# Optimization experiments

Hardware: AMD Instinct MI355X
Metric: run time of the kernel (lower is better)

The kernel has to match this reference:

```python
import jax, jax.numpy as jnp
import numpy as np

N_FFT = 64
FFT_STRIDE = 32
WINDOW_LENGTH = 1024
STRIDE = 128
FS = 2000.0


def _hann_nonperiodic(n):
    # torch.hann_window(n, periodic=False)
    k = jnp.arange(n, dtype=jnp.float32)
    return 0.5 * (1.0 - jnp.cos(2.0 * jnp.pi * k / (n - 1)))


def setup_inputs() -> dict:
    key = jax.random.key(0)
    inputs = jax.random.normal(key, (16, 16, 40000), dtype=jnp.float32)
    return {"inputs": inputs}


def reference(inputs) -> jnp.ndarray:
    B, C, T = inputs.shape
    num_freqs = N_FFT // 2 + 1
    window = _hann_nonperiodic(N_FFT)
    wnorm = jnp.linalg.norm(window)

    # --- STFT (center=False, onesided, complex), matching torch.stft ---
    x = inputs.reshape(B * C, T)
    num_frames = (T - N_FFT) // FFT_STRIDE + 1  # 1249
    frame_idx = jnp.arange(num_frames)[:, None] * FFT_STRIDE + jnp.arange(N_FFT)[None, :]
    frames = x[:, frame_idx] * window  # (BC, frames, n_fft)
    spec = jnp.fft.rfft(frames, axis=-1) / wnorm  # (BC, frames, F) complex64
    spec = jnp.swapaxes(spec, 1, 2)  # (BC, F, frames)

    # --- unfold over time frames into MPF windows ---
    ws = WINDOW_LENGTH // FFT_STRIDE  # 32
    step = STRIDE // FFT_STRIDE  # 4
    num_windows = (num_frames - ws) // step + 1  # 305
    widx = jnp.arange(num_windows)[:, None] * step + jnp.arange(ws)[None, :]
    spec_w = spec[:, :, widx]  # (BC, F, W, ws)
    spec_w = spec_w.reshape(B, C, num_freqs, num_windows, ws)
    spec_w = jnp.transpose(spec_w, (0, 3, 2, 1, 4))  # (B, W, F, C, ws)

    # --- cross-spectral density, |.|^2 ---
    csd = jnp.einsum("bwfcs,bwfds->bwfcd", spec_w, jnp.conj(spec_w)) / ws
    csd = csd.real ** 2 + csd.imag ** 2  # (B, W, F, C, C) real, PSD

    # --- log-eigen reconstruction ---
    eigvals, eigvecs = jnp.linalg.eigh(csd)
    eigvals = jnp.nan_to_num(jnp.log(eigvals), nan=0.0, neginf=0.0)
    out = (eigvecs * eigvals[..., None, :]) @ jnp.swapaxes(eigvecs, -1, -2)
    # (B, W, F, C, C) -> (B, F, C, C, W)
    return jnp.transpose(out, (0, 2, 3, 4, 1))
```

## Files before the change

kernel.cpp:

```cpp
#include <hip/hip_runtime.h>
#include <math.h>

#define NFRAMES 1249
#define NFREQ   33
#define NWIN    305
#define NCH     16
#define T_IN    40000
#define NSWEEP  8

__global__ __launch_bounds__(256) void kspec(const float* __restrict__ x,
                                             float2* __restrict__ spec) {
    __shared__ float2 twid[64];
    __shared__ float  win[64];
    int tid = threadIdx.x;
    if (tid < 64) {
        const float PI2 = 6.28318530717958647692f;
        float ang = (PI2 / 64.0f) * (float)tid;
        twid[tid] = make_float2(cosf(ang), -sinf(ang));
        float wv  = 0.5f * (1.0f - cosf((PI2 / 63.0f) * (float)tid));
        win[tid]  = wv * (1.0f / sqrtf(23.625f));
    }
    __syncthreads();

    int fl = tid & 15;
    int c  = tid >> 4;
    int b  = blockIdx.y;
    int frame = blockIdx.x * 16 + fl;
    if (frame >= NFRAMES) return;

    const float* xp = x + (size_t)(b * 16 + c) * T_IN + (size_t)frame * 32;
    float xw[64];
    #pragma unroll
    for (int k = 0; k < 16; k++) {
        float4 v = reinterpret_cast<const float4*>(xp)[k];
        xw[4*k+0] = v.x * win[4*k+0];
        xw[4*k+1] = v.y * win[4*k+1];
        xw[4*k+2] = v.z * win[4*k+2];
        xw[4*k+3] = v.w * win[4*k+3];
    }
    for (int f = 0; f < NFREQ; f++) {
        float re = 0.0f, im = 0.0f;
        #pragma unroll
        for (int n = 0; n < 64; n++) {
            float2 tw = twid[(f * n) & 63];
            re = fmaf(xw[n], tw.x, re);
            im = fmaf(xw[n], tw.y, im);
        }
        spec[((size_t)(b * NFREQ + f) * NFRAMES + frame) * NCH + c] = make_float2(re, im);
    }
}

__global__ __launch_bounds__(256) void keig(const float2* __restrict__ spec,
                                            float* __restrict__ outC, int direct) {
    __shared__ float Gs[16][16][17];
    __shared__ float Hs[16][16][17];
    int tid  = threadIdx.x;
    int lane = tid & 63;
    int matl = tid >> 4;
    int t    = tid & 15;
    int mat  = blockIdx.x * 16 + matl;
    int wwin = mat % NWIN;
    int bf   = mat / NWIN;

    const float2* zb = spec + ((size_t)bf * NFRAMES + (size_t)wwin * 4) * NCH;

    float cr[16], ci[16];
    #pragma unroll
    for (int c2 = 0; c2 < 16; c2++) { cr[c2] = 0.0f; ci[c2] = 0.0f; }
    for (int chunk = 0; chunk < 4; chunk++) {
        float zx[8], zy[8];
        #pragma unroll
        for (int s = 0; s < 8; s++) {
            float2 z = zb[(size_t)(chunk * 8 + s) * NCH + t];
            zx[s] = z.x; zy[s] = z.y;
        }
        #pragma unroll
        for (int c2 = 0; c2 < 16; c2++) {
            int src = (lane & 48) | c2;
            #pragma unroll
            for (int s = 0; s < 8; s++) {
                float zcx = __shfl(zx[s], src);
                float zcy = __shfl(zy[s], src);
                cr[c2] = fmaf(zcx, zx[s], fmaf(zcy, zy[s], cr[c2]));
                ci[c2] = fmaf(zcy, zx[s], fmaf(-zcx, zy[s], ci[c2]));
            }
        }
    }
    float a[16];
    #pragma unroll
    for (int c2 = 0; c2 < 16; c2++)
        a[c2] = (cr[c2] * cr[c2] + ci[c2] * ci[c2]) * (1.0f / 1024.0f);

    for (int sweep = 0; sweep < NSWEEP; sweep++) {
        for (int m = 1; m < 16; m++) {
            int pl = lane ^ m;
            float app = 0.0f;
            #pragma unroll
            for (int i = 0; i < 16; i++) app = fmaf(a[i], a[i], app);
            float aqq = __shfl(app, pl);
            float bcol[16];
            #pragma unroll
            for (int i = 0; i < 16; i++) bcol[i] = __shfl(a[i], pl);
            float apq = 0.0f;
            #pragma unroll
            for (int i = 0; i < 16; i++) apq = fmaf(a[i], bcol[i], apq);
            bool isP = t < (t ^ m);
            float npp = isP ? app : aqq;
            float nqq = isP ? aqq : app;
            if (apq * apq > npp * nqq * 1e-14f) {
                float tau = (nqq - npp) / (2.0f * apq);
                float tt  = copysignf(1.0f, tau) / (fabsf(tau) + sqrtf(fmaf(tau, tau, 1.0f)));
                float cc  = 1.0f / sqrtf(fmaf(tt, tt, 1.0f));
                float ss  = tt * cc;
                float se  = isP ? -ss : ss;
                #pragma unroll
                for (int i = 0; i < 16; i++) a[i] = fmaf(se, bcol[i], cc * a[i]);
            }
        }
    }

    float sqn = 0.0f;
    #pragma unroll
    for (int i = 0; i < 16; i++) sqn = fmaf(a[i], a[i], sqn);
    float wgt = 0.0f;
    if (sqn > 1e-30f) wgt = 0.5f * logf(sqn) / sqn;

    #pragma unroll
    for (int i = 0; i < 16; i++) {
        Gs[matl][t][i] = a[i];
        Hs[matl][t][i] = wgt * a[i];
    }
    __syncthreads();

    float acc[16];
    #pragma unroll
    for (int i = 0; i < 16; i++) acc[i] = 0.0f;
    #pragma unroll
    for (int j = 0; j < 16; j++) {
        float hjt = Hs[matl][j][t];
        #pragma unroll
        for (int i = 0; i < 16; i++) acc[i] = fmaf(Gs[matl][j][i], hjt, acc[i]);
    }

    if (!direct) {
        float* op = outC + (size_t)mat * 256;
        #pragma unroll
        for (int i = 0; i < 16; i++) op[i * 16 + t] = acc[i];
    } else {
        float* op = outC + (size_t)bf * 256 * NWIN + wwin;
        #pragma unroll
        for (int i = 0; i < 16; i++) op[(size_t)(i * 16 + t) * NWIN] = acc[i];
    }
}

__global__ __launch_bounds__(256) void ktrans(const float* __restrict__ in,
                                              float* __restrict__ out) {
    __shared__ float tile[32][33];
    int bf = blockIdx.z;
    const float* ip = in  + (size_t)bf * NWIN * 256;
    float*       op = out + (size_t)bf * 256 * NWIN;
    int tx = threadIdx.x, ty = threadIdx.y;
    int w0 = blockIdx.x * 32, cd0 = blockIdx.y * 32;
    #pragma unroll
    for (int r = 0; r < 32; r += 8) {
        int w = w0 + ty + r;
        if (w < NWIN) tile[ty + r][tx] = ip[(size_t)w * 256 + cd0 + tx];
    }
    __syncthreads();
    #pragma unroll
    for (int r = 0; r < 32; r += 8) {
        int cd = cd0 + ty + r;
        int w  = w0 + tx;
        if (w < NWIN) op[(size_t)cd * NWIN + w] = tile[tx][ty + r];
    }
}

extern "C" void kernel_launch(void* const* d_in, const int* in_sizes, int n_in,
                              void* d_out, int out_size, void* d_ws, size_t ws_size,
                              hipStream_t stream) {
    const float* x = (const float*)d_in[0];
    float* out = (float*)d_out;

    float2* spec = (float2*)d_ws;
    const size_t specBytes = (size_t)16 * NFREQ * NFRAMES * NCH * sizeof(float2);
    const size_t cBytes    = (size_t)161040 * 256 * sizeof(float);
    float* Cws = (float*)((char*)d_ws + specBytes);
    int full = (ws_size >= specBytes + cBytes) ? 1 : 0;

    kspec<<<dim3(79, 16), 256, 0, stream>>>(x, spec);
    if (full) {
        keig<<<dim3(10065), 256, 0, stream>>>(spec, Cws, 0);
        ktrans<<<dim3(10, 8, 528), dim3(32, 8), 0, stream>>>(Cws, out);
    } else {
        keig<<<dim3(10065), 256, 0, stream>>>(spec, out, 1);
    }
}
```

Baseline: 1.711 ms.

## Fuse output transpose into eigen kernel, add Jacobi early exit, fewer sweeps

The eigen kernel now writes the (B,F,C,C,W) layout directly through a shared-memory transpose. This removes the separate transpose kernel and the round trip through the intermediate workspace buffer. The Jacobi solver drops from 8 to 6 sweeps with a looser rotation threshold. It also exits early once no wavefront performs a rotation and updates the diagonal norm incrementally instead of recomputing it each pair. The 1/1024 scaling moves into the window constant. Fewer sweeps and the looser threshold risk lower eigen-decomposition accuracy, and the grid now pads the 305 windows per (b,f) up to 320.

```diff
diff --git a/kernel.cpp b/kernel.cpp
--- a/kernel.cpp
+++ b/kernel.cpp
@@ -6,7 +6,7 @@
 #define NWIN    305
 #define NCH     16
 #define T_IN    40000
-#define NSWEEP  8
+#define NSWEEP  6
 
 __global__ __launch_bounds__(256) void kspec(const float* __restrict__ x,
                                              float2* __restrict__ spec) {
@@ -18,7 +18,7 @@
         float ang = (PI2 / 64.0f) * (float)tid;
         twid[tid] = make_float2(cosf(ang), -sinf(ang));
         float wv  = 0.5f * (1.0f - cosf((PI2 / 63.0f) * (float)tid));
-        win[tid]  = wv * (1.0f / sqrtf(23.625f));
+        win[tid]  = wv * (1.0f / sqrtf(23.625f * 32.0f));
     }
     __syncthreads();
 
@@ -51,16 +51,16 @@
 }
 
 __global__ __launch_bounds__(256) void keig(const float2* __restrict__ spec,
-                                            float* __restrict__ outC, int direct) {
-    __shared__ float Gs[16][16][17];
-    __shared__ float Hs[16][16][17];
+                                            float* __restrict__ out) {
+    __shared__ float Gs[16 * 16 * 17];
+    __shared__ float wgts[16][16];
     int tid  = threadIdx.x;
     int lane = tid & 63;
     int matl = tid >> 4;
     int t    = tid & 15;
-    int mat  = blockIdx.x * 16 + matl;
-    int wwin = mat % NWIN;
-    int bf   = mat / NWIN;
+    int w0   = blockIdx.x * 16;
+    int bf   = blockIdx.y;
+    int wwin = min(w0 + matl, NWIN - 1);
 
     const float2* zb = spec + ((size_t)bf * NFRAMES + (size_t)wwin * 4) * NCH;
 
@@ -89,14 +89,16 @@
     float a[16];
     #pragma unroll
     for (int c2 = 0; c2 < 16; c2++)
-        a[c2] = (cr[c2] * cr[c2] + ci[c2] * ci[c2]) * (1.0f / 1024.0f);
+        a[c2] = fmaf(cr[c2], cr[c2], ci[c2] * ci[c2]);
 
+    #pragma unroll 1
     for (int sweep = 0; sweep < NSWEEP; sweep++) {
+        float app = 0.0f;
+        #pragma unroll
+        for (int i = 0; i < 16; i++) app = fmaf(a[i], a[i], app);
+        int any = 0;
         for (int m = 1; m < 16; m++) {
             int pl = lane ^ m;
-            float app = 0.0f;
-            #pragma unroll
-            for (int i = 0; i < 16; i++) app = fmaf(a[i], a[i], app);
             float aqq = __shfl(app, pl);
             float bcol[16];
             #pragma unroll
@@ -107,7 +109,7 @@
             bool isP = t < (t ^ m);
             float npp = isP ? app : aqq;
             float nqq = isP ? aqq : app;
-            if (apq * apq > npp * nqq * 1e-14f) {
+            if (apq * apq > npp * nqq * 1e-12f) {
                 float tau = (nqq - npp) / (2.0f * apq);
                 float tt  = copysignf(1.0f, tau) / (fabsf(tau) + sqrtf(fmaf(tau, tau, 1.0f)));
                 float cc  = 1.0f / sqrtf(fmaf(tt, tt, 1.0f));
@@ -115,8 +117,11 @@
                 float se  = isP ? -ss : ss;
                 #pragma unroll
                 for (int i = 0; i < 16; i++) a[i] = fmaf(se, bcol[i], cc * a[i]);
+                app = fmaf(isP ? -tt : tt, apq, app);
+                any = 1;
             }
         }
+        if (!__any(any)) break;
     }
 
     float sqn = 0.0f;
@@ -125,11 +130,10 @@
     float wgt = 0.0f;
     if (sqn > 1e-30f) wgt = 0.5f * logf(sqn) / sqn;
 
+    float* G = &Gs[0];
     #pragma unroll
-    for (int i = 0; i < 16; i++) {
-        Gs[matl][t][i] = a[i];
-        Hs[matl][t][i] = wgt * a[i];
-    }
+    for (int i = 0; i < 16; i++) G[(matl * 16 + t) * 17 + i] = a[i];
+    wgts[matl][t] = wgt;
     __syncthreads();
 
     float acc[16];
@@ -137,41 +141,26 @@
     for (int i = 0; i < 16; i++) acc[i] = 0.0f;
     #pragma unroll
     for (int j = 0; j < 16; j++) {
-        float hjt = Hs[matl][j][t];
+        float hjt = wgts[matl][j] * G[(matl * 16 + j) * 17 + t];
         #pragma unroll
-        for (int i = 0; i < 16; i++) acc[i] = fmaf(Gs[matl][j][i], hjt, acc[i]);
-    }
-
-    if (!direct) {
-        float* op = outC + (size_t)mat * 256;
-        #pragma unroll
-        for (int i = 0; i < 16; i++) op[i * 16 + t] = acc[i];
-    } else {
-        float* op = outC + (size_t)bf * 256 * NWIN + wwin;
-        #pragma unroll
-        for (int i = 0; i < 16; i++) op[(size_t)(i * 16 + t) * NWIN] = acc[i];
-    }
-}
-
-__global__ __launch_bounds__(256) void ktrans(const float* __restrict__ in,
-                                              float* __restrict__ out) {
-    __shared__ float tile[32][33];
-    int bf = blockIdx.z;
-    const float* ip = in  + (size_t)bf * NWIN * 256;
-    float*       op = out + (size_t)bf * 256 * NWIN;
-    int tx = threadIdx.x, ty = threadIdx.y;
-    int w0 = blockIdx.x * 32, cd0 = blockIdx.y * 32;
-    #pragma unroll
-    for (int r = 0; r < 32; r += 8) {
-        int w = w0 + ty + r;
-        if (w < NWIN) tile[ty + r][tx] = ip[(size_t)w * 256 + cd0 + tx];
+        for (int i = 0; i < 16; i++)
+            acc[i] = fmaf(G[(matl * 16 + j) * 17 + i], hjt, acc[i]);
     }
     __syncthreads();
+
     #pragma unroll
-    for (int r = 0; r < 32; r += 8) {
-        int cd = cd0 + ty + r;
-        int w  = w0 + tx;
-        if (w < NWIN) op[(size_t)cd * NWIN + w] = tile[tx][ty + r];
+    for (int i = 0; i < 16; i++) G[(i * 16 + t) * 17 + matl] = acc[i];
+    __syncthreads();
+
+    int w  = tid & 15;
+    int cdr = tid >> 4;
+    if (w0 + w < NWIN) {
+        float* op = out + (size_t)bf * (256 * NWIN) + (size_t)(w0 + w);
+        #pragma unroll
+        for (int k = 0; k < 16; k++) {
+            int cd = k * 16 + cdr;
+            op[(size_t)cd * NWIN] = G[cd * 17 + w];
+        }
     }
 }
 
@@ -180,18 +169,8 @@
                               hipStream_t stream) {
     const float* x = (const float*)d_in[0];
     float* out = (float*)d_out;
-
     float2* spec = (float2*)d_ws;
-    const size_t specBytes = (size_t)16 * NFREQ * NFRAMES * NCH * sizeof(float2);
-    const size_t cBytes    = (size_t)161040 * 256 * sizeof(float);
-    float* Cws = (float*)((char*)d_ws + specBytes);
-    int full = (ws_size >= specBytes + cBytes) ? 1 : 0;
 
     kspec<<<dim3(79, 16), 256, 0, stream>>>(x, spec);
-    if (full) {
-        keig<<<dim3(10065), 256, 0, stream>>>(spec, Cws, 0);
-        ktrans<<<dim3(10, 8, 528), dim3(32, 8), 0, stream>>>(Cws, out);
-    } else {
-        keig<<<dim3(10065), 256, 0, stream>>>(spec, out, 1);
-    }
+    keig<<<dim3(20, 528), 256, 0, stream>>>(spec, out);
 }
```

Result: faster. 1.402 ms (-18.1%).
